# Performance work log

Measured on AMD Instinct MI355X. Metric: run time of the kernel, lower is better.

## Reference

```python
import jax, jax.numpy as jnp
import numpy as np

HIDDEN = 2048
N_HEADS = 16
N_KV_HEADS = 4
HEAD_DIM = HIDDEN // N_HEADS  # 128
ROPE_THETA = 10000.0
BATCH = 2
SEQ = 2048


def setup_inputs() -> dict:
    key = jax.random.key(0)
    k1, k2, k3, k4, k5 = jax.random.split(key, 5)
    s = 0.02
    return {
        "hidden_states": jax.random.normal(k1, (BATCH, SEQ, HIDDEN), dtype=jnp.float32),
        "attention_mask": jnp.zeros((BATCH, 1, 1, SEQ), dtype=jnp.float32),
        "Wq": jax.random.normal(k2, (HIDDEN, N_HEADS * HEAD_DIM), dtype=jnp.float32) * s,
        "Wk": jax.random.normal(k3, (HIDDEN, N_KV_HEADS * HEAD_DIM), dtype=jnp.float32) * s,
        "Wv": jax.random.normal(k4, (HIDDEN, N_KV_HEADS * HEAD_DIM), dtype=jnp.float32) * s,
        "Wo": jax.random.normal(k5, (N_HEADS * HEAD_DIM, HIDDEN), dtype=jnp.float32) * s,
    }


def _rope_cos_sin(seq_len, dtype):
    inv_freq = 1.0 / (ROPE_THETA ** (jnp.arange(0, HEAD_DIM, 2, dtype=jnp.float32) / HEAD_DIM))
    t = jnp.arange(seq_len, dtype=jnp.float32)
    freqs = t[:, None] * inv_freq[None, :]            # [S, D/2]
    emb = jnp.concatenate([freqs, freqs], axis=-1)    # [S, D]
    cos = jnp.cos(emb)[None, None, :, :].astype(dtype)  # [1,1,S,D]
    sin = jnp.sin(emb)[None, None, :, :].astype(dtype)
    return cos, sin


def _apply_rope(x, cos, sin):
    # x: [B,H,S,D]; faithful to torch code: rotated = cat((-x[...,1::2], x[...,::2]), -1)
    x1 = x[..., ::2]
    x2 = x[..., 1::2]
    rotated = jnp.concatenate([-x2, x1], axis=-1)
    return x * cos + rotated * sin


def reference(hidden_states, attention_mask, Wq, Wk, Wv, Wo):
    B, S, _ = hidden_states.shape
    scale = HEAD_DIM ** -0.5

    q = (hidden_states @ Wq).reshape(B, S, N_HEADS, HEAD_DIM).transpose(0, 2, 1, 3)      # [B,H,S,D]
    k = (hidden_states @ Wk).reshape(B, S, N_KV_HEADS, HEAD_DIM).transpose(0, 2, 1, 3)   # [B,KV,S,D]
    v = (hidden_states @ Wv).reshape(B, S, N_KV_HEADS, HEAD_DIM).transpose(0, 2, 1, 3)

    cos, sin = _rope_cos_sin(S, hidden_states.dtype)
    q = _apply_rope(q, cos, sin)
    k = _apply_rope(k, cos, sin)

    rep = N_HEADS // N_KV_HEADS
    k = jnp.repeat(k, rep, axis=1)  # [B,H,S,D]
    v = jnp.repeat(v, rep, axis=1)

    scores = jnp.einsum("bhqd,bhkd->bhqk", q, k) * scale  # [B,H,S,S]
    causal = jnp.tril(jnp.ones((S, S), dtype=bool))[None, None]
    scores = jnp.where(causal, scores, -jnp.inf)
    scores = scores + attention_mask  # additive float mask, broadcast [B,1,1,S]

    attn = jax.nn.softmax(scores, axis=-1)
    out = jnp.einsum("bhqk,bhkd->bhqd", attn, v)           # [B,H,S,D]
    out = out.transpose(0, 2, 1, 3).reshape(B, S, N_HEADS * HEAD_DIM)
    return out @ Wo
```

## Files before the change

### kernel.cpp

```cpp
#include <hip/hip_runtime.h>
#include <hip/hip_bf16.h>

#define BATCH 2
#define SEQ   2048
#define NH    16
#define NKV   4
#define HD    128
#define KDIM  2048
#define MROWS 4096
#define NQKV  3072

typedef __attribute__((ext_vector_type(8))) short  s16x8;
typedef __attribute__((ext_vector_type(4))) short  s16x4;
typedef __attribute__((ext_vector_type(4))) float  f32x4;
typedef __attribute__((ext_vector_type(8))) __bf16 b16x8;

#define BARRIER_LDS() do { \
    asm volatile("s_waitcnt lgkmcnt(0)" ::: "memory"); \
    __builtin_amdgcn_s_barrier(); \
  } while (0)

__device__ __forceinline__ unsigned short f2bf(float f) {
  __hip_bfloat16 h = __float2bfloat16(f);
  return *reinterpret_cast<unsigned short*>(&h);
}
__device__ __forceinline__ float bf2f(unsigned short h) {
  union { unsigned int u; float f; } x; x.u = ((unsigned int)h) << 16;
  return x.f;
}

__device__ __forceinline__ f32x4 MFMA16(s16x8 a, s16x8 b, f32x4 c) {
  return __builtin_amdgcn_mfma_f32_16x16x32_bf16(
      __builtin_bit_cast(b16x8, a), __builtin_bit_cast(b16x8, b), c, 0, 0, 0);
}

__device__ __forceinline__ void gload_lds16(const void* g, void* lds) {
  __builtin_amdgcn_global_load_lds(
      (const __attribute__((address_space(1))) void*)g,
      (__attribute__((address_space(3))) void*)lds, 16, 0, 0);
}

__global__ __launch_bounds__(256) void prep_weights(
    const float* __restrict__ Wq, const float* __restrict__ Wk,
    const float* __restrict__ Wv, const float* __restrict__ Wo,
    unsigned short* __restrict__ BT, unsigned short* __restrict__ WoT) {
  __shared__ float tile[32][33];
  int bx = blockIdx.x;
  const float* W; unsigned short* WT; int Nd, nb;
  if (bx < 64)       { W = Wq; WT = BT;                          Nd = 2048; nb = bx; }
  else if (bx < 80)  { W = Wk; WT = BT + (size_t)2048 * KDIM;    Nd = 512;  nb = bx - 64; }
  else if (bx < 96)  { W = Wv; WT = BT + (size_t)2560 * KDIM;    Nd = 512;  nb = bx - 80; }
  else               { W = Wo; WT = WoT;                         Nd = 2048; nb = bx - 96; }
  int n0 = nb * 32, k0 = blockIdx.y * 32;
  int tx = threadIdx.x & 31, ty = threadIdx.x >> 5;
#pragma unroll
  for (int i = 0; i < 4; ++i)
    tile[ty + i * 8][tx] = W[(size_t)(k0 + ty + i * 8) * Nd + n0 + tx];
  __syncthreads();
#pragma unroll
  for (int i = 0; i < 4; ++i)
    WT[(size_t)(n0 + ty + i * 8) * KDIM + k0 + tx] = f2bf(tile[tx][ty + i * 8]);
}

__global__ __launch_bounds__(256) void conv_bf16(
    const float* __restrict__ X, unsigned short* __restrict__ Y) {
  int i = blockIdx.x * 256 + threadIdx.x;
  const float4 a = ((const float4*)X)[2 * i];
  const float4 b = ((const float4*)X)[2 * i + 1];
  s16x8 o;
  o[0] = (short)f2bf(a.x); o[1] = (short)f2bf(a.y);
  o[2] = (short)f2bf(a.z); o[3] = (short)f2bf(a.w);
  o[4] = (short)f2bf(b.x); o[5] = (short)f2bf(b.y);
  o[6] = (short)f2bf(b.z); o[7] = (short)f2bf(b.w);
  ((s16x8*)Y)[i] = o;
}

__global__ __launch_bounds__(256) void rope_table_kernel(float* __restrict__ tbl) {
  int i = blockIdx.x * 256 + threadIdx.x;
  int s = i >> 6, j = i & 63;
  float inv = powf(10000.0f, -(float)(2 * j) * (1.0f / 128.0f));
  float f = (float)s * inv;
  tbl[2 * i]     = cosf(f);
  tbl[2 * i + 1] = sinf(f);
}

__global__ __launch_bounds__(512, 2) void gemm_qkv(
    const unsigned short* __restrict__ A, const unsigned short* __restrict__ BT,
    unsigned short* __restrict__ Qo, unsigned short* __restrict__ Ko,
    unsigned short* __restrict__ Vo) {
  __shared__ __align__(16) unsigned short lds[4][2][8192];
  int tid = threadIdx.x, lane = tid & 63;
  int w = tid >> 6, wm = w >> 2, wn = w & 3;
  int lin = blockIdx.x;
  int swz = (lin & 7) * 24 + (lin >> 3);
  int bx = swz % 12, by = swz / 12;
  int m0 = by * 256, n0 = bx * 256;
  int fr = lane & 15, cg4 = lane >> 4, rg4 = (lane >> 4) * 4;

  int rS1 = tid >> 2,        cS1 = (tid & 3) ^ (rS1 & 3);
  int t2  = tid + 512;
  int rS2 = t2 >> 2,         cS2 = (t2 & 3) ^ (rS2 & 3);

  f32x4 acc[8][4] = {};

#pragma unroll
  for (int kt = 0; kt < 2; ++kt) {
    gload_lds16(A + (size_t)(m0 + rS1) * KDIM + kt * 32 + cS1 * 8,
                (char*)&lds[kt][0][0] + (size_t)tid * 16);
    gload_lds16(A + (size_t)(m0 + rS2) * KDIM + kt * 32 + cS2 * 8,
                (char*)&lds[kt][0][0] + (size_t)t2 * 16);
    gload_lds16(BT + (size_t)(n0 + rS1) * KDIM + kt * 32 + cS1 * 8,
                (char*)&lds[kt][1][0] + (size_t)tid * 16);
    gload_lds16(BT + (size_t)(n0 + rS2) * KDIM + kt * 32 + cS2 * 8,
                (char*)&lds[kt][1][0] + (size_t)t2 * 16);
  }

  for (int kt = 0; kt < KDIM / 32; ++kt) {
    int buf = kt & 3;
    asm volatile("s_waitcnt vmcnt(4)" ::: "memory");
    __builtin_amdgcn_s_barrier();

    const unsigned short* lA = &lds[buf][0][0];
    const unsigned short* lB = &lds[buf][1][0];
    s16x8 bfr[4], afr[4];
#pragma unroll
    for (int nf = 0; nf < 4; ++nf) {
      int rb = wn * 64 + nf * 16 + fr;
      bfr[nf] = *(const s16x8*)(lB + rb * 32 + (cg4 ^ (rb & 3)) * 8);
    }
#pragma unroll
    for (int mf = 0; mf < 4; ++mf) {
      int ra = wm * 128 + mf * 16 + fr;
      afr[mf] = *(const s16x8*)(lA + ra * 32 + (cg4 ^ (ra & 3)) * 8);
    }
    if (kt + 2 < KDIM / 32) {
      int nb = (kt + 2) & 3, ko = (kt + 2) * 32;
      gload_lds16(A + (size_t)(m0 + rS1) * KDIM + ko + cS1 * 8,
                  (char*)&lds[nb][0][0] + (size_t)tid * 16);
      gload_lds16(A + (size_t)(m0 + rS2) * KDIM + ko + cS2 * 8,
                  (char*)&lds[nb][0][0] + (size_t)t2 * 16);
    }
    __builtin_amdgcn_s_setprio(1);
#pragma unroll
    for (int mf = 0; mf < 4; ++mf)
#pragma unroll
      for (int nf = 0; nf < 4; ++nf)
        acc[mf][nf] = MFMA16(afr[mf], bfr[nf], acc[mf][nf]);
    __builtin_amdgcn_s_setprio(0);
#pragma unroll
    for (int mf = 0; mf < 4; ++mf) {
      int ra = wm * 128 + (mf + 4) * 16 + fr;
      afr[mf] = *(const s16x8*)(lA + ra * 32 + (cg4 ^ (ra & 3)) * 8);
    }
    if (kt + 2 < KDIM / 32) {
      int nb = (kt + 2) & 3, ko = (kt + 2) * 32;
      gload_lds16(BT + (size_t)(n0 + rS1) * KDIM + ko + cS1 * 8,
                  (char*)&lds[nb][1][0] + (size_t)tid * 16);
      gload_lds16(BT + (size_t)(n0 + rS2) * KDIM + ko + cS2 * 8,
                  (char*)&lds[nb][1][0] + (size_t)t2 * 16);
    }
    __builtin_amdgcn_s_setprio(1);
#pragma unroll
    for (int mf = 0; mf < 4; ++mf)
#pragma unroll
      for (int nf = 0; nf < 4; ++nf)
        acc[mf + 4][nf] = MFMA16(afr[mf], bfr[nf], acc[mf + 4][nf]);
    __builtin_amdgcn_s_setprio(0);
  }

  int rbase = m0 + wm * 128 + rg4;
#pragma unroll
  for (int nf = 0; nf < 4; ++nf) {
    int gn = n0 + wn * 64 + nf * 16 + fr;
    if (gn < 2048) {
      int hh = gn >> 7, d = gn & 127;
#pragma unroll
      for (int mf = 0; mf < 8; ++mf)
#pragma unroll
        for (int r = 0; r < 4; ++r) {
          int grow = rbase + mf * 16 + r;
          int bb = grow >> 11, ss = grow & 2047;
          Qo[((size_t)(bb * NH + hh) * SEQ + ss) * HD + d] = f2bf(acc[mf][nf][r]);
        }
    } else if (gn < 2560) {
      int c = gn - 2048, kvh = c >> 7, d = c & 127;
#pragma unroll
      for (int mf = 0; mf < 8; ++mf)
#pragma unroll
        for (int r = 0; r < 4; ++r) {
          int grow = rbase + mf * 16 + r;
          int bb = grow >> 11, ss = grow & 2047;
          Ko[((size_t)(bb * NKV + kvh) * SEQ + ss) * HD + d] = f2bf(acc[mf][nf][r]);
        }
    } else {
      int c = gn - 2560, kvh = c >> 7, d = c & 127;
#pragma unroll
      for (int mf = 0; mf < 8; ++mf) {
        int grow0 = rbase + mf * 16;
        int bb = grow0 >> 11, ss = grow0 & 2047;
        s16x4 pk;
#pragma unroll
        for (int r = 0; r < 4; ++r) pk[r] = (short)f2bf(acc[mf][nf][r]);
        *(s16x4*)(Vo + ((size_t)(bb * NKV + kvh) * HD + d) * SEQ + ss) = pk;
      }
    }
  }
}

__global__ __launch_bounds__(512, 1) void gemm_out(
    const unsigned short* __restrict__ A, const unsigned short* __restrict__ BT,
    float* __restrict__ C) {
  __shared__ __align__(16) unsigned short ldsA[4][8192];
  __shared__ __align__(16) unsigned short ldsB[4][4096];
  int tid = threadIdx.x, lane = tid & 63;
  int w = tid >> 6, wm = w >> 2, wn = w & 3;
  int lin = blockIdx.x;
  int swz = (lin & 7) * 32 + (lin >> 3);
  int bx = swz % 16, by = swz / 16;
  int m0 = by * 256, n0 = bx * 128;
  int fr = lane & 15, cg4 = lane >> 4, rg4 = (lane >> 4) * 4;

  int rS1 = tid >> 2,  cS1 = (tid & 3) ^ (rS1 & 3);
  int t2  = tid + 512;
  int rS2 = t2 >> 2,   cS2 = (t2 & 3) ^ (rS2 & 3);
  int rB  = tid >> 2,  cB  = (tid & 3) ^ (rB & 3);
  bool doB = (tid < 512);

  f32x4 acc[8][2] = {};

#pragma unroll
  for (int kt = 0; kt < 2; ++kt) {
    gload_lds16(A + (size_t)(m0 + rS1) * KDIM + kt * 32 + cS1 * 8,
                (char*)&ldsA[kt][0] + (size_t)tid * 16);
    gload_lds16(A + (size_t)(m0 + rS2) * KDIM + kt * 32 + cS2 * 8,
                (char*)&ldsA[kt][0] + (size_t)t2 * 16);
    gload_lds16(BT + (size_t)(n0 + rB) * KDIM + kt * 32 + cB * 8,
                (char*)&ldsB[kt][0] + (size_t)tid * 16);
  }

  for (int kt = 0; kt < KDIM / 32; ++kt) {
    int buf = kt & 3;
    asm volatile("s_waitcnt vmcnt(3)" ::: "memory");
    __builtin_amdgcn_s_barrier();

    const unsigned short* lA = &ldsA[buf][0];
    const unsigned short* lB = &ldsB[buf][0];
    s16x8 bfr[2], afr[4];
#pragma unroll
    for (int nf = 0; nf < 2; ++nf) {
      int rb = wn * 32 + nf * 16 + fr;
      bfr[nf] = *(const s16x8*)(lB + rb * 32 + (cg4 ^ (rb & 3)) * 8);
    }
#pragma unroll
    for (int mf = 0; mf < 4; ++mf) {
      int ra = wm * 128 + mf * 16 + fr;
      afr[mf] = *(const s16x8*)(lA + ra * 32 + (cg4 ^ (ra & 3)) * 8);
    }
    if (kt + 2 < KDIM / 32) {
      int nb = (kt + 2) & 3, ko = (kt + 2) * 32;
      gload_lds16(A + (size_t)(m0 + rS1) * KDIM + ko + cS1 * 8,
                  (char*)&ldsA[nb][0] + (size_t)tid * 16);
      gload_lds16(A + (size_t)(m0 + rS2) * KDIM + ko + cS2 * 8,
                  (char*)&ldsA[nb][0] + (size_t)t2 * 16);
    }
    __builtin_amdgcn_s_setprio(1);
#pragma unroll
    for (int mf = 0; mf < 4; ++mf)
#pragma unroll
      for (int nf = 0; nf < 2; ++nf)
        acc[mf][nf] = MFMA16(afr[mf], bfr[nf], acc[mf][nf]);
    __builtin_amdgcn_s_setprio(0);
#pragma unroll
    for (int mf = 0; mf < 4; ++mf) {
      int ra = wm * 128 + (mf + 4) * 16 + fr;
      afr[mf] = *(const s16x8*)(lA + ra * 32 + (cg4 ^ (ra & 3)) * 8);
    }
    if (kt + 2 < KDIM / 32) {
      int nb = (kt + 2) & 3, ko = (kt + 2) * 32;
      gload_lds16(BT + (size_t)(n0 + rB) * KDIM + ko + cB * 8,
                  (char*)&ldsB[nb][0] + (size_t)tid * 16);
    }
    __builtin_amdgcn_s_setprio(1);
#pragma unroll
    for (int mf = 0; mf < 4; ++mf)
#pragma unroll
      for (int nf = 0; nf < 2; ++nf)
        acc[mf + 4][nf] = MFMA16(afr[mf], bfr[nf], acc[mf + 4][nf]);
    __builtin_amdgcn_s_setprio(0);
  }

  int rbase = m0 + wm * 128 + rg4;
#pragma unroll
  for (int nf = 0; nf < 2; ++nf) {
    int gn = n0 + wn * 32 + nf * 16 + fr;
#pragma unroll
    for (int mf = 0; mf < 8; ++mf)
#pragma unroll
      for (int r = 0; r < 4; ++r)
        C[(size_t)(rbase + mf * 16 + r) * 2048 + gn] = acc[mf][nf][r];
  }
}

__global__ __launch_bounds__(256) void rope2(
    unsigned short* __restrict__ Qx, unsigned short* __restrict__ Kx,
    const float* __restrict__ tbl) {
  __shared__ __align__(16) unsigned short xs[32][136];
  int tid = threadIdx.x;
  int bid = blockIdx.x;
  unsigned short* X;
  size_t r0;
  if (bid < 2048) { X = Qx; r0 = (size_t)bid * 32; }
  else            { X = Kx; r0 = (size_t)(bid - 2048) * 32; }
#pragma unroll
  for (int i = 0; i < 2; ++i) {
    int idx = tid + i * 256;
    int pr = idx >> 4, seg = idx & 15;
    *(s16x8*)(&xs[pr][seg * 8]) = *(const s16x8*)(X + (r0 + pr) * 128 + seg * 8);
  }
  __syncthreads();
  int pr = tid >> 3, jb = (tid & 7) * 8;
  size_t row = r0 + pr;
  int s = (int)(row & (SEQ - 1));
  s16x8 o0, o1;
#pragma unroll
  for (int j0 = 0; j0 < 8; ++j0) {
    int j = jb + j0;
    float c  = tbl[(s * 64 + j) * 2];
    float sn = tbl[(s * 64 + j) * 2 + 1];
    float xj   = bf2f(xs[pr][j]);
    float xj64 = bf2f(xs[pr][j + 64]);
    float x2j  = bf2f(xs[pr][2 * j]);
    float x2j1 = bf2f(xs[pr][2 * j + 1]);
    o0[j0] = (short)f2bf(xj * c - x2j1 * sn);
    o1[j0] = (short)f2bf(xj64 * c + x2j * sn);
  }
  unsigned short* xp = X + row * 128;
  *(s16x8*)(xp + jb)      = o0;
  *(s16x8*)(xp + 64 + jb) = o1;
}

__global__ __launch_bounds__(256, 2) void attn_fwd(
    const unsigned short* __restrict__ Q, const unsigned short* __restrict__ K,
    const unsigned short* __restrict__ VT, const float* __restrict__ mask,
    unsigned short* __restrict__ O) {
  __shared__ __align__(16) unsigned short kt_[2][64][136];
  __shared__ __align__(16) unsigned short vt_[2][128][68];
  __shared__ __align__(16) unsigned short pt_[4][16][36];

  int tid = threadIdx.x, lane = tid & 63, w = tid >> 6;
  int l = blockIdx.x;
  int grp = l & 7, slot = l >> 3;
  int hloc = slot & 3, qt = 31 - (slot >> 2);
  int b = grp >> 2, kvh = grp & 3, h = kvh * 4 + hloc;
  int qbase = qt * 64;
  int qw = qbase + w * 16;
  int fr = lane & 15, g = lane >> 4, kg = g * 8, rg = g * 4;

  const unsigned short* Qb = Q + (size_t)(b * NH + h) * SEQ * HD;
  const unsigned short* Kb = K + (size_t)(b * NKV + kvh) * SEQ * HD;
  const unsigned short* Vb = VT + (size_t)(b * NKV + kvh) * HD * SEQ;
  const float* mb = mask + (size_t)b * SEQ;

  int krow = tid >> 4, kpos = (tid & 15) * 8;
  const float sc2 = 0.12751744584812722f;
  const float L2E = 1.44269504088896f;
  int bS = b * SEQ;
  int ntiles = qt + 1;

  s16x8 aq[4];
#pragma unroll
  for (int dc = 0; dc < 4; ++dc)
    aq[dc] = *(const s16x8*)(Qb + (size_t)(qw + fr) * HD + dc * 32 + kg);

  f32x4 oacc[8] = {};
  float m_r = -3e38f, l_r = 0.f;

  s16x8 kreg[4], vreg[4];
#pragma unroll
  for (int i = 0; i < 4; ++i)
    kreg[i] = *(const s16x8*)(Kb + (size_t)(krow + i * 16) * HD + kpos);
#pragma unroll
  for (int i = 0; i < 4; ++i) {
    int c = tid + 256 * i;
    vreg[i] = *(const s16x8*)(Vb + (size_t)(c >> 3) * SEQ + (c & 7) * 8);
  }
#pragma unroll
  for (int i = 0; i < 4; ++i)
    *(s16x8*)(&kt_[0][krow + i * 16][kpos]) = kreg[i];
#pragma unroll
  for (int i = 0; i < 4; ++i) {
    int c = tid + 256 * i;
    *(s16x8*)(&vt_[0][c >> 3][(c & 7) * 8]) = vreg[i];
  }
  if (ntiles > 1) {
#pragma unroll
    for (int i = 0; i < 4; ++i)
      kreg[i] = *(const s16x8*)(Kb + (size_t)(64 + krow + i * 16) * HD + kpos);
#pragma unroll
    for (int i = 0; i < 4; ++i) {
      int c = tid + 256 * i;
      vreg[i] = *(const s16x8*)(Vb + (size_t)(c >> 3) * SEQ + 64 + (c & 7) * 8);
    }
  }
  BARRIER_LDS();

  for (int t = 0; t < ntiles; ++t) {
    int kv0 = t * 64;
    int cur = t & 1;
    bool diag = (t == qt);

    if (t + 1 < ntiles) {
#pragma unroll
      for (int i = 0; i < 4; ++i)
        *(s16x8*)(&kt_[cur ^ 1][krow + i * 16][kpos]) = kreg[i];
#pragma unroll
      for (int i = 0; i < 4; ++i) {
        int c = tid + 256 * i;
        *(s16x8*)(&vt_[cur ^ 1][c >> 3][(c & 7) * 8]) = vreg[i];
      }
      if (t + 2 < ntiles) {
#pragma unroll
        for (int i = 0; i < 4; ++i)
          kreg[i] = *(const s16x8*)(Kb + (size_t)(kv0 + 128 + krow + i * 16) * HD + kpos);
#pragma unroll
        for (int i = 0; i < 4; ++i) {
          int c = tid + 256 * i;
          vreg[i] = *(const s16x8*)(Vb + (size_t)(c >> 3) * SEQ + kv0 + 128 + (c & 7) * 8);
        }
      }
    }

    f32x4 sf[4];
    __builtin_amdgcn_s_setprio(1);
#pragma unroll
    for (int mk = 0; mk < 4; ++mk) {
      s16x8 ak[4];
#pragma unroll
      for (int dc = 0; dc < 4; ++dc)
        ak[dc] = *(const s16x8*)(&kt_[cur][mk * 16 + fr][dc * 32 + kg]);
      sf[mk] = f32x4{0.f, 0.f, 0.f, 0.f};
#pragma unroll
      for (int dc = 0; dc < 4; ++dc)
        sf[mk] = MFMA16(ak[dc], aq[dc], sf[mk]);
    }
    __builtin_amdgcn_s_setprio(0);

#pragma unroll
    for (int mk = 0; mk < 4; ++mk) {
      float4 mv = *(const float4*)(mb + kv0 + mk * 16 + rg);
      float mvr[4] = {mv.x * L2E, mv.y * L2E, mv.z * L2E, mv.w * L2E};
      if (diag) {
#pragma unroll
        for (int r = 0; r < 4; ++r) {
          int kv = kv0 + mk * 16 + rg + r;
          float v = sf[mk][r] * sc2 + mvr[r];
          sf[mk][r] = (kv <= qw + fr) ? v : -3e38f;
        }
      } else {
#pragma unroll
        for (int r = 0; r < 4; ++r)
          sf[mk][r] = sf[mk][r] * sc2 + mvr[r];
      }
    }

    float pm01a = fmaxf(sf[0][0], sf[0][1]), pm01b = fmaxf(sf[0][2], sf[0][3]);
    float pm11a = fmaxf(sf[1][0], sf[1][1]), pm11b = fmaxf(sf[1][2], sf[1][3]);
    float pm21a = fmaxf(sf[2][0], sf[2][1]), pm21b = fmaxf(sf[2][2], sf[2][3]);
    float pm31a = fmaxf(sf[3][0], sf[3][1]), pm31b = fmaxf(sf[3][2], sf[3][3]);
    float pm0 = fmaxf(pm01a, pm01b), pm1 = fmaxf(pm11a, pm11b);
    float pm2 = fmaxf(pm21a, pm21b), pm3 = fmaxf(pm31a, pm31b);
    float pm = fmaxf(fmaxf(pm0, pm1), fmaxf(pm2, pm3));
    pm = fmaxf(pm, __shfl_xor(pm, 16, 64));
    pm = fmaxf(pm, __shfl_xor(pm, 32, 64));
    if (!__all(pm - m_r <= 8.0f)) {
      float mo = m_r;
      float mn = fmaxf(mo, pm);
      float al = exp2f(mo - mn);
      m_r = mn;
      l_r *= al;
#pragma unroll
      for (int r = 0; r < 4; ++r) {
        float ar = __shfl(al, rg + r, 16);
#pragma unroll
        for (int od = 0; od < 8; ++od) oacc[od][r] *= ar;
      }
    }
    float rs = 0.f;
#pragma unroll
    for (int mk = 0; mk < 4; ++mk)
#pragma unroll
      for (int r = 0; r < 4; ++r) {
        float ppv = exp2f(sf[mk][r] - m_r);
        sf[mk][r] = ppv;
        rs += ppv;
      }
    rs += __shfl_xor(rs, 16, 64);
    rs += __shfl_xor(rs, 32, 64);
    l_r += rs;

#pragma unroll
    for (int kk = 0; kk < 2; ++kk) {
#pragma unroll
      for (int mh = 0; mh < 2; ++mh) {
        int mk = kk * 2 + mh;
        s16x4 pk;
#pragma unroll
        for (int r = 0; r < 4; ++r) pk[r] = (short)f2bf(sf[mk][r]);
        *(s16x4*)(&pt_[w][fr][mh * 16 + rg]) = pk;
      }
      s16x8 ap = *(const s16x8*)(&pt_[w][fr][kg]);
      __builtin_amdgcn_s_setprio(1);
#pragma unroll
      for (int od = 0; od < 8; ++od) {
        s16x8 bv = *(const s16x8*)(&vt_[cur][od * 16 + fr][kk * 32 + kg]);
        oacc[od] = MFMA16(ap, bv, oacc[od]);
      }
      __builtin_amdgcn_s_setprio(0);
    }

    BARRIER_LDS();
  }

  float iv = 1.0f / l_r;
  float ivr[4];
#pragma unroll
  for (int r = 0; r < 4; ++r) ivr[r] = __shfl(iv, rg + r, 16);
#pragma unroll
  for (int r = 0; r < 4; ++r) {
    unsigned short* op = O + (size_t)(bS + qw + rg + r) * 2048 + h * 128 + fr;
#pragma unroll
    for (int od = 0; od < 8; ++od)
      op[od * 16] = f2bf(oacc[od][r] * ivr[r]);
  }
}

extern "C" void kernel_launch(void* const* d_in, const int* in_sizes, int n_in,
                              void* d_out, int out_size, void* d_ws, size_t ws_size,
                              hipStream_t stream) {
  const float* hidden = (const float*)d_in[0];
  const float* mask   = (const float*)d_in[1];
  const float* Wq     = (const float*)d_in[2];
  const float* Wk     = (const float*)d_in[3];
  const float* Wv     = (const float*)d_in[4];
  const float* Wo     = (const float*)d_in[5];
  float* out = (float*)d_out;

  char* ws = (char*)d_ws;
  unsigned short* BT  = (unsigned short*)(ws);
  unsigned short* WoT = (unsigned short*)(ws + 12582912);
  unsigned short* Qb  = (unsigned short*)(ws + 20971520);
  unsigned short* Kb  = (unsigned short*)(ws + 37748736);
  unsigned short* VT  = (unsigned short*)(ws + 41943040);
  unsigned short* AO  = (unsigned short*)(ws + 46137344);
  float*          tbl = (float*)(ws + 62914560);
  unsigned short* Ab  = AO;

  conv_bf16<<<MROWS * KDIM / (256 * 8), 256, 0, stream>>>(hidden, Ab);
  prep_weights<<<dim3(160, 64), 256, 0, stream>>>(Wq, Wk, Wv, Wo, BT, WoT);
  rope_table_kernel<<<512, 256, 0, stream>>>(tbl);

  gemm_qkv<<<dim3(192), 512, 0, stream>>>(Ab, BT, Qb, Kb, VT);
  rope2<<<dim3(2048 + 512), 256, 0, stream>>>(Qb, Kb, tbl);
  attn_fwd<<<dim3(1024), 256, 0, stream>>>(Qb, Kb, VT, mask, AO);
  gemm_out<<<dim3(256), 512, 0, stream>>>(AO, WoT, out);
}
```

Baseline: 220.5 us.

## Fuse RoPE into QKV GEMM epilogue and merge prep kernels into one launch

Result: faster. 204.2 us (-7.4%).

```diff
diff --git a/kernel.cpp b/kernel.cpp
--- a/kernel.cpp
+++ b/kernel.cpp
@@ -40,55 +40,57 @@
       (__attribute__((address_space(3))) void*)lds, 16, 0, 0);
 }
 
-__global__ __launch_bounds__(256) void prep_weights(
+__global__ __launch_bounds__(256) void prep_all(
+    const float* __restrict__ hidden,
     const float* __restrict__ Wq, const float* __restrict__ Wk,
     const float* __restrict__ Wv, const float* __restrict__ Wo,
-    unsigned short* __restrict__ BT, unsigned short* __restrict__ WoT) {
+    unsigned short* __restrict__ Ab, unsigned short* __restrict__ BT,
+    unsigned short* __restrict__ WoT, float* __restrict__ tbl) {
   __shared__ float tile[32][33];
-  int bx = blockIdx.x;
-  const float* W; unsigned short* WT; int Nd, nb;
-  if (bx < 64)       { W = Wq; WT = BT;                          Nd = 2048; nb = bx; }
-  else if (bx < 80)  { W = Wk; WT = BT + (size_t)2048 * KDIM;    Nd = 512;  nb = bx - 64; }
-  else if (bx < 96)  { W = Wv; WT = BT + (size_t)2560 * KDIM;    Nd = 512;  nb = bx - 80; }
-  else               { W = Wo; WT = WoT;                         Nd = 2048; nb = bx - 96; }
-  int n0 = nb * 32, k0 = blockIdx.y * 32;
-  int tx = threadIdx.x & 31, ty = threadIdx.x >> 5;
-#pragma unroll
-  for (int i = 0; i < 4; ++i)
-    tile[ty + i * 8][tx] = W[(size_t)(k0 + ty + i * 8) * Nd + n0 + tx];
-  __syncthreads();
-#pragma unroll
-  for (int i = 0; i < 4; ++i)
-    WT[(size_t)(n0 + ty + i * 8) * KDIM + k0 + tx] = f2bf(tile[tx][ty + i * 8]);
-}
-
-__global__ __launch_bounds__(256) void conv_bf16(
-    const float* __restrict__ X, unsigned short* __restrict__ Y) {
-  int i = blockIdx.x * 256 + threadIdx.x;
-  const float4 a = ((const float4*)X)[2 * i];
-  const float4 b = ((const float4*)X)[2 * i + 1];
-  s16x8 o;
-  o[0] = (short)f2bf(a.x); o[1] = (short)f2bf(a.y);
-  o[2] = (short)f2bf(a.z); o[3] = (short)f2bf(a.w);
-  o[4] = (short)f2bf(b.x); o[5] = (short)f2bf(b.y);
-  o[6] = (short)f2bf(b.z); o[7] = (short)f2bf(b.w);
-  ((s16x8*)Y)[i] = o;
-}
-
-__global__ __launch_bounds__(256) void rope_table_kernel(float* __restrict__ tbl) {
-  int i = blockIdx.x * 256 + threadIdx.x;
-  int s = i >> 6, j = i & 63;
-  float inv = powf(10000.0f, -(float)(2 * j) * (1.0f / 128.0f));
-  float f = (float)s * inv;
-  tbl[2 * i]     = cosf(f);
-  tbl[2 * i + 1] = sinf(f);
+  int bid = blockIdx.x;
+  if (bid < 10240) {
+    int sub = bid % 160, ky = bid / 160;
+    const float* W; unsigned short* WT; int Nd, nb;
+    if (sub < 64)       { W = Wq; WT = BT;                       Nd = 2048; nb = sub; }
+    else if (sub < 80)  { W = Wk; WT = BT + (size_t)2048 * KDIM; Nd = 512;  nb = sub - 64; }
+    else if (sub < 96)  { W = Wv; WT = BT + (size_t)2560 * KDIM; Nd = 512;  nb = sub - 80; }
+    else                { W = Wo; WT = WoT;                      Nd = 2048; nb = sub - 96; }
+    int n0 = nb * 32, k0 = ky * 32;
+    int tx = threadIdx.x & 31, ty = threadIdx.x >> 5;
+#pragma unroll
+    for (int i = 0; i < 4; ++i)
+      tile[ty + i * 8][tx] = W[(size_t)(k0 + ty + i * 8) * Nd + n0 + tx];
+    __syncthreads();
+#pragma unroll
+    for (int i = 0; i < 4; ++i)
+      WT[(size_t)(n0 + ty + i * 8) * KDIM + k0 + tx] = f2bf(tile[tx][ty + i * 8]);
+  } else if (bid < 14336) {
+    int i = (bid - 10240) * 256 + threadIdx.x;
+    const float4 a = ((const float4*)hidden)[2 * i];
+    const float4 b = ((const float4*)hidden)[2 * i + 1];
+    s16x8 o;
+    o[0] = (short)f2bf(a.x); o[1] = (short)f2bf(a.y);
+    o[2] = (short)f2bf(a.z); o[3] = (short)f2bf(a.w);
+    o[4] = (short)f2bf(b.x); o[5] = (short)f2bf(b.y);
+    o[6] = (short)f2bf(b.z); o[7] = (short)f2bf(b.w);
+    ((s16x8*)Ab)[i] = o;
+  } else {
+    int i = (bid - 14336) * 256 + threadIdx.x;
+    int s = i >> 6, j = i & 63;
+    float inv = powf(10000.0f, -(float)(2 * j) * (1.0f / 128.0f));
+    float f = (float)s * inv;
+    tbl[2 * i]     = cosf(f);
+    tbl[2 * i + 1] = sinf(f);
+  }
 }
 
 __global__ __launch_bounds__(512, 2) void gemm_qkv(
     const unsigned short* __restrict__ A, const unsigned short* __restrict__ BT,
+    const float* __restrict__ tbl,
     unsigned short* __restrict__ Qo, unsigned short* __restrict__ Ko,
     unsigned short* __restrict__ Vo) {
-  __shared__ __align__(16) unsigned short lds[4][2][8192];
+  __shared__ __align__(16) unsigned short lds_[66560];
+#define RING(buf, ab) (lds_ + (((buf) * 2 + (ab)) << 13))
   int tid = threadIdx.x, lane = tid & 63;
   int w = tid >> 6, wm = w >> 2, wn = w & 3;
   int lin = blockIdx.x;
@@ -106,22 +108,24 @@
 #pragma unroll
   for (int kt = 0; kt < 2; ++kt) {
     gload_lds16(A + (size_t)(m0 + rS1) * KDIM + kt * 32 + cS1 * 8,
-                (char*)&lds[kt][0][0] + (size_t)tid * 16);
+                (char*)RING(kt, 0) + (size_t)tid * 16);
     gload_lds16(A + (size_t)(m0 + rS2) * KDIM + kt * 32 + cS2 * 8,
-                (char*)&lds[kt][0][0] + (size_t)t2 * 16);
+                (char*)RING(kt, 0) + (size_t)t2 * 16);
     gload_lds16(BT + (size_t)(n0 + rS1) * KDIM + kt * 32 + cS1 * 8,
-                (char*)&lds[kt][1][0] + (size_t)tid * 16);
+                (char*)RING(kt, 1) + (size_t)tid * 16);
     gload_lds16(BT + (size_t)(n0 + rS2) * KDIM + kt * 32 + cS2 * 8,
-                (char*)&lds[kt][1][0] + (size_t)t2 * 16);
-  }
-
-  for (int kt = 0; kt < KDIM / 32; ++kt) {
+                (char*)RING(kt, 1) + (size_t)t2 * 16);
+  }
+
+  const int NK = KDIM / 32;
+  for (int kt = 0; kt < NK; ++kt) {
     int buf = kt & 3;
-    asm volatile("s_waitcnt vmcnt(4)" ::: "memory");
+    if (kt == NK - 1) asm volatile("s_waitcnt vmcnt(0)" ::: "memory");
+    else              asm volatile("s_waitcnt vmcnt(4)" ::: "memory");
     __builtin_amdgcn_s_barrier();
 
-    const unsigned short* lA = &lds[buf][0][0];
-    const unsigned short* lB = &lds[buf][1][0];
+    const unsigned short* lA = RING(buf, 0);
+    const unsigned short* lB = RING(buf, 1);
     s16x8 bfr[4], afr[4];
 #pragma unroll
     for (int nf = 0; nf < 4; ++nf) {
@@ -133,12 +137,12 @@
       int ra = wm * 128 + mf * 16 + fr;
       afr[mf] = *(const s16x8*)(lA + ra * 32 + (cg4 ^ (ra & 3)) * 8);
     }
-    if (kt + 2 < KDIM / 32) {
+    if (kt + 2 < NK) {
       int nb = (kt + 2) & 3, ko = (kt + 2) * 32;
       gload_lds16(A + (size_t)(m0 + rS1) * KDIM + ko + cS1 * 8,
-                  (char*)&lds[nb][0][0] + (size_t)tid * 16);
+                  (char*)RING(nb, 0) + (size_t)tid * 16);
       gload_lds16(A + (size_t)(m0 + rS2) * KDIM + ko + cS2 * 8,
-                  (char*)&lds[nb][0][0] + (size_t)t2 * 16);
+                  (char*)RING(nb, 0) + (size_t)t2 * 16);
     }
     __builtin_amdgcn_s_setprio(1);
 #pragma unroll
@@ -152,12 +156,12 @@
       int ra = wm * 128 + (mf + 4) * 16 + fr;
       afr[mf] = *(const s16x8*)(lA + ra * 32 + (cg4 ^ (ra & 3)) * 8);
     }
-    if (kt + 2 < KDIM / 32) {
+    if (kt + 2 < NK) {
       int nb = (kt + 2) & 3, ko = (kt + 2) * 32;
       gload_lds16(BT + (size_t)(n0 + rS1) * KDIM + ko + cS1 * 8,
-                  (char*)&lds[nb][1][0] + (size_t)tid * 16);
+                  (char*)RING(nb, 1) + (size_t)tid * 16);
       gload_lds16(BT + (size_t)(n0 + rS2) * KDIM + ko + cS2 * 8,
-                  (char*)&lds[nb][1][0] + (size_t)t2 * 16);
+                  (char*)RING(nb, 1) + (size_t)t2 * 16);
     }
     __builtin_amdgcn_s_setprio(1);
 #pragma unroll
@@ -168,31 +172,66 @@
     __builtin_amdgcn_s_setprio(0);
   }
 
-  int rbase = m0 + wm * 128 + rg4;
-#pragma unroll
-  for (int nf = 0; nf < 4; ++nf) {
-    int gn = n0 + wn * 64 + nf * 16 + fr;
-    if (gn < 2048) {
-      int hh = gn >> 7, d = gn & 127;
-#pragma unroll
-      for (int mf = 0; mf < 8; ++mf)
-#pragma unroll
-        for (int r = 0; r < 4; ++r) {
-          int grow = rbase + mf * 16 + r;
-          int bb = grow >> 11, ss = grow & 2047;
-          Qo[((size_t)(bb * NH + hh) * SEQ + ss) * HD + d] = f2bf(acc[mf][nf][r]);
-        }
-    } else if (gn < 2560) {
-      int c = gn - 2048, kvh = c >> 7, d = c & 127;
-#pragma unroll
-      for (int mf = 0; mf < 8; ++mf)
-#pragma unroll
-        for (int r = 0; r < 4; ++r) {
-          int grow = rbase + mf * 16 + r;
-          int bb = grow >> 11, ss = grow & 2047;
-          Ko[((size_t)(bb * NKV + kvh) * SEQ + ss) * HD + d] = f2bf(acc[mf][nf][r]);
-        }
-    } else {
+  if (bx < 10) {
+    BARRIER_LDS();
+    unsigned short* sc_ = lds_;
+#pragma unroll
+    for (int mf = 0; mf < 8; ++mf)
+#pragma unroll
+      for (int nf = 0; nf < 4; ++nf)
+#pragma unroll
+        for (int r = 0; r < 4; ++r)
+          sc_[(wm * 128 + mf * 16 + rg4 + r) * 260 + wn * 64 + nf * 16 + fr] =
+              f2bf(acc[mf][nf][r]);
+    BARRIER_LDS();
+
+#pragma unroll
+    for (int i = 0; i < 8; ++i) {
+      int t = tid + 512 * i;
+      int row = t >> 4, rem = t & 15;
+      int hl = rem >> 3, j0 = (rem & 7) * 8;
+      int grow = m0 + row, bb = grow >> 11, ss = grow & 2047;
+      const unsigned short* xb = sc_ + row * 260 + hl * 128;
+      s16x8 xj  = *(const s16x8*)(xb + j0);
+      s16x8 xj6 = *(const s16x8*)(xb + 64 + j0);
+      s16x8 x2a = *(const s16x8*)(xb + 2 * j0);
+      s16x8 x2b = *(const s16x8*)(xb + 2 * j0 + 8);
+      const float* tb = tbl + ((size_t)ss * 64 + j0) * 2;
+      union { float4 v[4]; float a[16]; } cs;
+      cs.v[0] = *(const float4*)(tb);
+      cs.v[1] = *(const float4*)(tb + 4);
+      cs.v[2] = *(const float4*)(tb + 8);
+      cs.v[3] = *(const float4*)(tb + 12);
+      s16x8 o0, o1;
+#pragma unroll
+      for (int k = 0; k < 8; ++k) {
+        float c  = cs.a[2 * k];
+        float sn = cs.a[2 * k + 1];
+        float xjf  = bf2f((unsigned short)xj[k]);
+        float xj6f = bf2f((unsigned short)xj6[k]);
+        float x2j  = (2 * k < 8) ? bf2f((unsigned short)x2a[2 * k])
+                                 : bf2f((unsigned short)x2b[2 * k - 8]);
+        float x2j1 = (2 * k + 1 < 8) ? bf2f((unsigned short)x2a[2 * k + 1])
+                                     : bf2f((unsigned short)x2b[2 * k + 1 - 8]);
+        o0[k] = (short)f2bf(xjf * c - x2j1 * sn);
+        o1[k] = (short)f2bf(xj6f * c + x2j * sn);
+      }
+      unsigned short* dstp;
+      if (bx < 8) {
+        int hh = bx * 2 + hl;
+        dstp = Qo + ((size_t)(bb * NH + hh) * SEQ + ss) * HD;
+      } else {
+        int kvh = (bx - 8) * 2 + hl;
+        dstp = Ko + ((size_t)(bb * NKV + kvh) * SEQ + ss) * HD;
+      }
+      *(s16x8*)(dstp + j0)      = o0;
+      *(s16x8*)(dstp + 64 + j0) = o1;
+    }
+  } else {
+    int rbase = m0 + wm * 128 + rg4;
+#pragma unroll
+    for (int nf = 0; nf < 4; ++nf) {
+      int gn = n0 + wn * 64 + nf * 16 + fr;
       int c = gn - 2560, kvh = c >> 7, d = c & 127;
 #pragma unroll
       for (int mf = 0; mf < 8; ++mf) {
@@ -205,6 +244,7 @@
       }
     }
   }
+#undef RING
 }
 
 __global__ __launch_bounds__(512, 1) void gemm_out(
@@ -224,7 +264,6 @@
   int t2  = tid + 512;
   int rS2 = t2 >> 2,   cS2 = (t2 & 3) ^ (rS2 & 3);
   int rB  = tid >> 2,  cB  = (tid & 3) ^ (rB & 3);
-  bool doB = (tid < 512);
 
   f32x4 acc[8][2] = {};
 
@@ -238,9 +277,11 @@
                 (char*)&ldsB[kt][0] + (size_t)tid * 16);
   }
 
-  for (int kt = 0; kt < KDIM / 32; ++kt) {
+  const int NK = KDIM / 32;
+  for (int kt = 0; kt < NK; ++kt) {
     int buf = kt & 3;
-    asm volatile("s_waitcnt vmcnt(3)" ::: "memory");
+    if (kt == NK - 1) asm volatile("s_waitcnt vmcnt(0)" ::: "memory");
+    else              asm volatile("s_waitcnt vmcnt(3)" ::: "memory");
     __builtin_amdgcn_s_barrier();
 
     const unsigned short* lA = &ldsA[buf][0];
@@ -256,7 +297,7 @@
       int ra = wm * 128 + mf * 16 + fr;
       afr[mf] = *(const s16x8*)(lA + ra * 32 + (cg4 ^ (ra & 3)) * 8);
     }
-    if (kt + 2 < KDIM / 32) {
+    if (kt + 2 < NK) {
       int nb = (kt + 2) & 3, ko = (kt + 2) * 32;
       gload_lds16(A + (size_t)(m0 + rS1) * KDIM + ko + cS1 * 8,
                   (char*)&ldsA[nb][0] + (size_t)tid * 16);
@@ -275,7 +316,7 @@
       int ra = wm * 128 + (mf + 4) * 16 + fr;
       afr[mf] = *(const s16x8*)(lA + ra * 32 + (cg4 ^ (ra & 3)) * 8);
     }
-    if (kt + 2 < KDIM / 32) {
+    if (kt + 2 < NK) {
       int nb = (kt + 2) & 3, ko = (kt + 2) * 32;
       gload_lds16(BT + (size_t)(n0 + rB) * KDIM + ko + cB * 8,
                   (char*)&ldsB[nb][0] + (size_t)tid * 16);
@@ -299,44 +340,6 @@
       for (int r = 0; r < 4; ++r)
         C[(size_t)(rbase + mf * 16 + r) * 2048 + gn] = acc[mf][nf][r];
   }
-}
-
-__global__ __launch_bounds__(256) void rope2(
-    unsigned short* __restrict__ Qx, unsigned short* __restrict__ Kx,
-    const float* __restrict__ tbl) {
-  __shared__ __align__(16) unsigned short xs[32][136];
-  int tid = threadIdx.x;
-  int bid = blockIdx.x;
-  unsigned short* X;
-  size_t r0;
-  if (bid < 2048) { X = Qx; r0 = (size_t)bid * 32; }
-  else            { X = Kx; r0 = (size_t)(bid - 2048) * 32; }
-#pragma unroll
-  for (int i = 0; i < 2; ++i) {
-    int idx = tid + i * 256;
-    int pr = idx >> 4, seg = idx & 15;
-    *(s16x8*)(&xs[pr][seg * 8]) = *(const s16x8*)(X + (r0 + pr) * 128 + seg * 8);
-  }
-  __syncthreads();
-  int pr = tid >> 3, jb = (tid & 7) * 8;
-  size_t row = r0 + pr;
-  int s = (int)(row & (SEQ - 1));
-  s16x8 o0, o1;
-#pragma unroll
-  for (int j0 = 0; j0 < 8; ++j0) {
-    int j = jb + j0;
-    float c  = tbl[(s * 64 + j) * 2];
-    float sn = tbl[(s * 64 + j) * 2 + 1];
-    float xj   = bf2f(xs[pr][j]);
-    float xj64 = bf2f(xs[pr][j + 64]);
-    float x2j  = bf2f(xs[pr][2 * j]);
-    float x2j1 = bf2f(xs[pr][2 * j + 1]);
-    o0[j0] = (short)f2bf(xj * c - x2j1 * sn);
-    o1[j0] = (short)f2bf(xj64 * c + x2j * sn);
-  }
-  unsigned short* xp = X + row * 128;
-  *(s16x8*)(xp + jb)      = o0;
-  *(s16x8*)(xp + 64 + jb) = o1;
 }
 
 __global__ __launch_bounds__(256, 2) void attn_fwd(
@@ -555,12 +558,8 @@
   float*          tbl = (float*)(ws + 62914560);
   unsigned short* Ab  = AO;
 
-  conv_bf16<<<MROWS * KDIM / (256 * 8), 256, 0, stream>>>(hidden, Ab);
-  prep_weights<<<dim3(160, 64), 256, 0, stream>>>(Wq, Wk, Wv, Wo, BT, WoT);
-  rope_table_kernel<<<512, 256, 0, stream>>>(tbl);
-
-  gemm_qkv<<<dim3(192), 512, 0, stream>>>(Ab, BT, Qb, Kb, VT);
-  rope2<<<dim3(2048 + 512), 256, 0, stream>>>(Qb, Kb, tbl);
+  prep_all<<<dim3(14848), 256, 0, stream>>>(hidden, Wq, Wk, Wv, Wo, Ab, BT, WoT, tbl);
+  gemm_qkv<<<dim3(192), 512, 0, stream>>>(Ab, BT, tbl, Qb, Kb, VT);
   attn_fwd<<<dim3(1024), 256, 0, stream>>>(Qb, Kb, VT, mask, AO);
   gemm_out<<<dim3(256), 512, 0, stream>>>(AO, WoT, out);
 }
```
